# Kernel tuning notes

Hardware: AMD Instinct MI355X
Metric: run time of the kernel (lower is better)

Reference implementation:

```python
import jax, jax.numpy as jnp
import numpy as np

B, X_DIM, Y_DIM, HIDDEN = 512, 768, 128, 1024
H2 = HIDDEN // 2


def setup_inputs() -> dict:
    key = jax.random.key(0)
    ks = jax.random.split(key, 10)
    s_in = 1.0 / np.sqrt(X_DIM)
    s_h = 1.0 / np.sqrt(H2)
    return {
        "x_samples": jax.random.normal(ks[0], (B, X_DIM), jnp.float32),
        "y_samples": jax.random.normal(ks[1], (B, Y_DIM), jnp.float32),
        "w1_mu": jax.random.uniform(ks[2], (X_DIM, H2), jnp.float32, -s_in, s_in),
        "b1_mu": jax.random.uniform(ks[3], (H2,), jnp.float32, -s_in, s_in),
        "w2_mu": jax.random.uniform(ks[4], (H2, Y_DIM), jnp.float32, -s_h, s_h),
        "b2_mu": jax.random.uniform(ks[5], (Y_DIM,), jnp.float32, -s_h, s_h),
        "w1_lv": jax.random.uniform(ks[6], (X_DIM, H2), jnp.float32, -s_in, s_in),
        "b1_lv": jax.random.uniform(ks[7], (H2,), jnp.float32, -s_in, s_in),
        "w2_lv": jax.random.uniform(ks[8], (H2, Y_DIM), jnp.float32, -s_h, s_h),
        "b2_lv": jax.random.uniform(ks[9], (Y_DIM,), jnp.float32, -s_h, s_h),
    }


def reference(x_samples, y_samples, w1_mu, b1_mu, w2_mu, b2_mu,
              w1_lv, b1_lv, w2_lv, b2_lv):
    batch = y_samples.shape[0]
    # p_mu / p_logvar MLP heads
    mu = jax.nn.relu(x_samples @ w1_mu + b1_mu) @ w2_mu + b2_mu          # [B, Y]
    logvar = jnp.tanh(jax.nn.relu(x_samples @ w1_lv + b1_lv) @ w2_lv + b2_lv)  # [B, Y]

    inv_var = jnp.exp(-logvar)
    # positive: diagonal Gaussian log-prob of y_i under p(.|x_i), up to const
    positive = (-0.5 * (mu - y_samples) ** 2 * inv_var - 0.5 * logvar).sum(-1)  # [B]

    # pairwise log-probs: row i = params from x_i, col j = sample y_j
    mu_1 = mu[:, None, :]            # [B, 1, Y]
    lv_1 = logvar[:, None, :]        # [B, 1, Y]
    y_1 = y_samples[None, :, :]      # [1, B, Y]
    all_probs = (-0.5 * (y_1 - mu_1) ** 2 * jnp.exp(-lv_1) - 0.5 * lv_1).sum(-1)  # [B, B]

    # Faithful replication of the torch broadcasting: diag_mask is [B, B, 1],
    # so all_probs + diag_mask broadcasts to [B, B, B], then logsumexp over dim 0.
    diag_mask = (jnp.eye(batch, dtype=all_probs.dtype) * -20.0)[:, :, None]  # [B, B, 1]
    logits = all_probs + diag_mask                                           # [B, B, B]
    negative = jax.scipy.special.logsumexp(logits, axis=0) - jnp.log(batch - 1.0)  # [B, B]

    return (positive - negative).mean()
```

## Files before the change

### kernel.cpp

```cpp
#include <hip/hip_runtime.h>
#include <math.h>

#define BSZ   512
#define XD    768
#define YD    128
#define H2D   512

__global__ __launch_bounds__(256, 2) void layer1_kernel(
    const float* __restrict__ x,
    const float* __restrict__ w1_mu, const float* __restrict__ w1_lv,
    const float* __restrict__ y,
    float* __restrict__ p1,
    double* __restrict__ Sy, double* __restrict__ Sy2,
    double* __restrict__ accum, unsigned int* __restrict__ counter)
{
    __shared__ float As[16][68];
    __shared__ float Bs[16][68];
    const int t = threadIdx.x;

    if (blockIdx.z == 4) {
        const int id = blockIdx.x + 8 * blockIdx.y;
        if (id >= 16) return;
        const int dl = t & 7;
        const int g  = t >> 3;
        const int d  = id * 8 + dl;
        float s = 0.f, s2 = 0.f;
        for (int i = g * 16; i < g * 16 + 16; ++i) {
            const float v = y[i * YD + d];
            s += v; s2 += v * v;
        }
        float* shs  = &As[0][0];
        float* shs2 = &Bs[0][0];
        shs[t] = s; shs2[t] = s2;
        __syncthreads();
        if (t < 8) {
            double S = 0.0, S2 = 0.0;
            #pragma unroll
            for (int gg = 0; gg < 32; ++gg) {
                S += (double)shs[gg * 8 + t]; S2 += (double)shs2[gg * 8 + t];
            }
            Sy[id * 8 + t] = S; Sy2[id * 8 + t] = S2;
        } else if (id == 0 && t == 8)  { accum[0] = 0.0; }
        else if (id == 0 && t == 9)  { accum[1] = 0.0; }
        else if (id == 0 && t == 10) { *counter = 0u; }
        return;
    }

    const int bz     = blockIdx.z;
    const int branch = bz >> 1;
    const int ks     = bz & 1;
    const float* __restrict__ W = branch ? w1_lv : w1_mu;
    float* __restrict__ out = p1 + (size_t)bz * (BSZ * H2D);

    const int m0 = blockIdx.x * 64;
    const int n0 = blockIdx.y * 64;
    const int tx = t & 15;
    const int ty = t >> 4;

    const int am  = t >> 2;
    const int akq = (t & 3) << 2;
    const int bkk = t >> 4;
    const int bnq = (t & 15) << 2;

    const int kbase = ks * 384;
    float acc[4][4] = {};

    float4 a_pref = *(const float4*)&x[(m0 + am) * XD + kbase + akq];
    float4 b_pref = *(const float4*)&W[(kbase + bkk) * H2D + n0 + bnq];

    for (int kt = 0; kt < 384; kt += 16) {
        __syncthreads();
        As[akq + 0][am] = a_pref.x;
        As[akq + 1][am] = a_pref.y;
        As[akq + 2][am] = a_pref.z;
        As[akq + 3][am] = a_pref.w;
        *(float4*)&Bs[bkk][bnq] = b_pref;
        __syncthreads();
        if (kt + 16 < 384) {
            const int kn = kbase + kt + 16;
            a_pref = *(const float4*)&x[(m0 + am) * XD + kn + akq];
            b_pref = *(const float4*)&W[(kn + bkk) * H2D + n0 + bnq];
        }
        #pragma unroll
        for (int k = 0; k < 16; ++k) {
            const float4 av = *(const float4*)&As[k][ty * 4];
            const float4 bv = *(const float4*)&Bs[k][tx * 4];
            acc[0][0] += av.x*bv.x; acc[0][1] += av.x*bv.y; acc[0][2] += av.x*bv.z; acc[0][3] += av.x*bv.w;
            acc[1][0] += av.y*bv.x; acc[1][1] += av.y*bv.y; acc[1][2] += av.y*bv.z; acc[1][3] += av.y*bv.w;
            acc[2][0] += av.z*bv.x; acc[2][1] += av.z*bv.y; acc[2][2] += av.z*bv.z; acc[2][3] += av.z*bv.w;
            acc[3][0] += av.w*bv.x; acc[3][1] += av.w*bv.y; acc[3][2] += av.w*bv.z; acc[3][3] += av.w*bv.w;
        }
    }

    #pragma unroll
    for (int i = 0; i < 4; ++i) {
        const float4 o = make_float4(acc[i][0], acc[i][1], acc[i][2], acc[i][3]);
        *(float4*)&out[(m0 + ty * 4 + i) * H2D + n0 + tx * 4] = o;
    }
}

__global__ __launch_bounds__(256, 2) void layer2_kernel(
    const float* __restrict__ p1,
    const float* __restrict__ b1_mu, const float* __restrict__ b1_lv,
    const float* __restrict__ w2_mu, const float* __restrict__ w2_lv,
    float* __restrict__ p2)
{
    __shared__ float As[16][68];
    __shared__ float Bs[16][68];
    const int t = threadIdx.x;

    const int branch = blockIdx.z >> 3;
    const int ks     = blockIdx.z & 7;
    const float* __restrict__ pa = p1 + (size_t)(branch * 2 + 0) * (BSZ * H2D);
    const float* __restrict__ pb = p1 + (size_t)(branch * 2 + 1) * (BSZ * H2D);
    const float* __restrict__ b1 = branch ? b1_lv : b1_mu;
    const float* __restrict__ W  = branch ? w2_lv : w2_mu;
    float* __restrict__ out = p2 + (size_t)blockIdx.z * (BSZ * YD);

    const int m0 = blockIdx.x * 64;
    const int n0 = blockIdx.y * 64;
    const int tx = t & 15;
    const int ty = t >> 4;

    const int am  = t >> 2;
    const int akq = (t & 3) << 2;
    const int bkk = t >> 4;
    const int bnq = (t & 15) << 2;

    const int kbase = ks * 64;
    float acc[4][4] = {};

    float4 pa4 = *(const float4*)&pa[(m0 + am) * H2D + kbase + akq];
    float4 pb4 = *(const float4*)&pb[(m0 + am) * H2D + kbase + akq];
    float4 bb4 = *(const float4*)&b1[kbase + akq];
    float4 w4  = *(const float4*)&W[(kbase + bkk) * YD + n0 + bnq];

    for (int kt = 0; kt < 64; kt += 16) {
        __syncthreads();
        As[akq + 0][am] = fmaxf(pa4.x + pb4.x + bb4.x, 0.f);
        As[akq + 1][am] = fmaxf(pa4.y + pb4.y + bb4.y, 0.f);
        As[akq + 2][am] = fmaxf(pa4.z + pb4.z + bb4.z, 0.f);
        As[akq + 3][am] = fmaxf(pa4.w + pb4.w + bb4.w, 0.f);
        *(float4*)&Bs[bkk][bnq] = w4;
        __syncthreads();
        if (kt + 16 < 64) {
            const int kn = kbase + kt + 16;
            pa4 = *(const float4*)&pa[(m0 + am) * H2D + kn + akq];
            pb4 = *(const float4*)&pb[(m0 + am) * H2D + kn + akq];
            bb4 = *(const float4*)&b1[kn + akq];
            w4  = *(const float4*)&W[(kn + bkk) * YD + n0 + bnq];
        }
        #pragma unroll
        for (int k = 0; k < 16; ++k) {
            const float4 av = *(const float4*)&As[k][ty * 4];
            const float4 bv = *(const float4*)&Bs[k][tx * 4];
            acc[0][0] += av.x*bv.x; acc[0][1] += av.x*bv.y; acc[0][2] += av.x*bv.z; acc[0][3] += av.x*bv.w;
            acc[1][0] += av.y*bv.x; acc[1][1] += av.y*bv.y; acc[1][2] += av.y*bv.z; acc[1][3] += av.y*bv.w;
            acc[2][0] += av.z*bv.x; acc[2][1] += av.z*bv.y; acc[2][2] += av.z*bv.z; acc[2][3] += av.z*bv.w;
            acc[3][0] += av.w*bv.x; acc[3][1] += av.w*bv.y; acc[3][2] += av.w*bv.z; acc[3][3] += av.w*bv.w;
        }
    }

    #pragma unroll
    for (int i = 0; i < 4; ++i) {
        const float4 o = make_float4(acc[i][0], acc[i][1], acc[i][2], acc[i][3]);
        *(float4*)&out[(m0 + ty * 4 + i) * YD + n0 + tx * 4] = o;
    }
}

__global__ __launch_bounds__(256) void reduce_kernel(
    const float* __restrict__ p2, const float* __restrict__ y,
    const float* __restrict__ b2_mu, const float* __restrict__ b2_lv,
    const double* __restrict__ Sy, const double* __restrict__ Sy2,
    double* __restrict__ accum, unsigned int* __restrict__ counter,
    float* __restrict__ outp)
{
    const int NE = BSZ * YD;
    const int e  = blockIdx.x * 256 + threadIdx.x;
    const int d  = e & (YD - 1);

    float mu = b2_mu[d];
    float lp = b2_lv[d];
    #pragma unroll
    for (int s = 0; s < 8; ++s) {
        mu += p2[s * NE + e];
        lp += p2[(8 + s) * NE + e];
    }
    const float lv = tanhf(lp);
    const float iv = expf(-lv);
    const float dm = mu - y[e];

    double pos = -0.5 * (double)dm * (double)dm * (double)iv - 0.5 * (double)lv;
    double ap  = (double)iv * (-0.5 * Sy2[d] + (double)mu * Sy[d]
                               - 256.0 * (double)mu * (double)mu)
               - 256.0 * (double)lv;

    #pragma unroll
    for (int off = 32; off > 0; off >>= 1) {
        pos += __shfl_down(pos, off);
        ap  += __shfl_down(ap, off);
    }
    __shared__ double sp[4];
    __shared__ double sa[4];
    const int lane = threadIdx.x & 63;
    const int wv   = threadIdx.x >> 6;
    if (lane == 0) { sp[wv] = pos; sa[wv] = ap; }
    __syncthreads();
    if (threadIdx.x == 0) {
        atomicAdd(&accum[0], sp[0] + sp[1] + sp[2] + sp[3]);
        atomicAdd(&accum[1], sa[0] + sa[1] + sa[2] + sa[3]);
        __threadfence();
        const unsigned int old = atomicAdd(counter, 1u);
        if (old == 255u) {
            const double P = atomicAdd(&accum[0], 0.0);
            const double A = atomicAdd(&accum[1], 0.0);
            const double C = log1p(exp(-20.0) / 511.0);
            outp[0] = (float)(P / 512.0 - A / 262144.0 - C);
        }
    }
}

extern "C" void kernel_launch(void* const* d_in, const int* in_sizes, int n_in,
                              void* d_out, int out_size, void* d_ws, size_t ws_size,
                              hipStream_t stream) {
    const float* x     = (const float*)d_in[0];
    const float* y     = (const float*)d_in[1];
    const float* w1_mu = (const float*)d_in[2];
    const float* b1_mu = (const float*)d_in[3];
    const float* w2_mu = (const float*)d_in[4];
    const float* b2_mu = (const float*)d_in[5];
    const float* w1_lv = (const float*)d_in[6];
    const float* b1_lv = (const float*)d_in[7];
    const float* w2_lv = (const float*)d_in[8];
    const float* b2_lv = (const float*)d_in[9];

    char* ws = (char*)d_ws;
    float*  p1 = (float*)(ws);
    float*  p2 = (float*)(ws + (size_t)4 * BSZ * H2D * 4);
    double* Sy = (double*)(ws + (size_t)4 * BSZ * H2D * 4
                              + (size_t)16 * BSZ * YD * 4);
    double* Sy2 = Sy + YD;
    double* accum = Sy2 + YD;
    unsigned int* counter = (unsigned int*)(accum + 2);

    layer1_kernel<<<dim3(8, 8, 5), 256, 0, stream>>>(
        x, w1_mu, w1_lv, y, p1, Sy, Sy2, accum, counter);
    layer2_kernel<<<dim3(8, 2, 16), 256, 0, stream>>>(
        p1, b1_mu, b1_lv, w2_mu, w2_lv, p2);
    reduce_kernel<<<256, 256, 0, stream>>>(
        p2, y, b2_mu, b2_lv, Sy, Sy2, accum, counter, (float*)d_out);
}
```

Baseline: 110.5 us.

## Split layer-1 K dimension four ways and spread final atomics over slots

Layer 1 now splits the 768-long reduction into four 192-long partial products per branch instead of two, doubling the block count from 256 to 512 to fill more compute units. Layer 2 sums four partial planes instead of two when applying bias and ReLU, so it reads more intermediate data. The reduce kernel spreads its double-precision atomic adds across 16 slots to cut contention, and the last block sums the slots. The cost is a larger workspace and more global traffic for the intermediate buffers.

```diff
diff --git a/kernel.cpp b/kernel.cpp
--- a/kernel.cpp
+++ b/kernel.cpp
@@ -18,7 +18,7 @@
     __shared__ float Bs[16][68];
     const int t = threadIdx.x;
 
-    if (blockIdx.z == 4) {
+    if (blockIdx.z == 8) {
         const int id = blockIdx.x + 8 * blockIdx.y;
         if (id >= 16) return;
         const int dl = t & 7;
@@ -40,15 +40,14 @@
                 S += (double)shs[gg * 8 + t]; S2 += (double)shs2[gg * 8 + t];
             }
             Sy[id * 8 + t] = S; Sy2[id * 8 + t] = S2;
-        } else if (id == 0 && t == 8)  { accum[0] = 0.0; }
-        else if (id == 0 && t == 9)  { accum[1] = 0.0; }
-        else if (id == 0 && t == 10) { *counter = 0u; }
+        } else if (id == 0 && t >= 8 && t < 40) { accum[t - 8] = 0.0; }
+        else if (id == 0 && t == 40)            { *counter = 0u; }
         return;
     }
 
     const int bz     = blockIdx.z;
-    const int branch = bz >> 1;
-    const int ks     = bz & 1;
+    const int branch = bz >> 2;
+    const int ks     = bz & 3;
     const float* __restrict__ W = branch ? w1_lv : w1_mu;
     float* __restrict__ out = p1 + (size_t)bz * (BSZ * H2D);
 
@@ -62,13 +61,13 @@
     const int bkk = t >> 4;
     const int bnq = (t & 15) << 2;
 
-    const int kbase = ks * 384;
+    const int kbase = ks * 192;
     float acc[4][4] = {};
 
     float4 a_pref = *(const float4*)&x[(m0 + am) * XD + kbase + akq];
     float4 b_pref = *(const float4*)&W[(kbase + bkk) * H2D + n0 + bnq];
 
-    for (int kt = 0; kt < 384; kt += 16) {
+    for (int kt = 0; kt < 192; kt += 16) {
         __syncthreads();
         As[akq + 0][am] = a_pref.x;
         As[akq + 1][am] = a_pref.y;
@@ -76,7 +75,7 @@
         As[akq + 3][am] = a_pref.w;
         *(float4*)&Bs[bkk][bnq] = b_pref;
         __syncthreads();
-        if (kt + 16 < 384) {
+        if (kt + 16 < 192) {
             const int kn = kbase + kt + 16;
             a_pref = *(const float4*)&x[(m0 + am) * XD + kn + akq];
             b_pref = *(const float4*)&W[(kn + bkk) * H2D + n0 + bnq];
@@ -111,8 +110,10 @@
 
     const int branch = blockIdx.z >> 3;
     const int ks     = blockIdx.z & 7;
-    const float* __restrict__ pa = p1 + (size_t)(branch * 2 + 0) * (BSZ * H2D);
-    const float* __restrict__ pb = p1 + (size_t)(branch * 2 + 1) * (BSZ * H2D);
+    const float* __restrict__ pa = p1 + (size_t)(branch * 4 + 0) * (BSZ * H2D);
+    const float* __restrict__ pb = p1 + (size_t)(branch * 4 + 1) * (BSZ * H2D);
+    const float* __restrict__ pc = p1 + (size_t)(branch * 4 + 2) * (BSZ * H2D);
+    const float* __restrict__ pd = p1 + (size_t)(branch * 4 + 3) * (BSZ * H2D);
     const float* __restrict__ b1 = branch ? b1_lv : b1_mu;
     const float* __restrict__ W  = branch ? w2_lv : w2_mu;
     float* __restrict__ out = p2 + (size_t)blockIdx.z * (BSZ * YD);
@@ -132,21 +133,25 @@
 
     float4 pa4 = *(const float4*)&pa[(m0 + am) * H2D + kbase + akq];
     float4 pb4 = *(const float4*)&pb[(m0 + am) * H2D + kbase + akq];
+    float4 pc4 = *(const float4*)&pc[(m0 + am) * H2D + kbase + akq];
+    float4 pd4 = *(const float4*)&pd[(m0 + am) * H2D + kbase + akq];
     float4 bb4 = *(const float4*)&b1[kbase + akq];
     float4 w4  = *(const float4*)&W[(kbase + bkk) * YD + n0 + bnq];
 
     for (int kt = 0; kt < 64; kt += 16) {
         __syncthreads();
-        As[akq + 0][am] = fmaxf(pa4.x + pb4.x + bb4.x, 0.f);
-        As[akq + 1][am] = fmaxf(pa4.y + pb4.y + bb4.y, 0.f);
-        As[akq + 2][am] = fmaxf(pa4.z + pb4.z + bb4.z, 0.f);
-        As[akq + 3][am] = fmaxf(pa4.w + pb4.w + bb4.w, 0.f);
+        As[akq + 0][am] = fmaxf(pa4.x + pb4.x + pc4.x + pd4.x + bb4.x, 0.f);
+        As[akq + 1][am] = fmaxf(pa4.y + pb4.y + pc4.y + pd4.y + bb4.y, 0.f);
+        As[akq + 2][am] = fmaxf(pa4.z + pb4.z + pc4.z + pd4.z + bb4.z, 0.f);
+        As[akq + 3][am] = fmaxf(pa4.w + pb4.w + pc4.w + pd4.w + bb4.w, 0.f);
         *(float4*)&Bs[bkk][bnq] = w4;
         __syncthreads();
         if (kt + 16 < 64) {
             const int kn = kbase + kt + 16;
             pa4 = *(const float4*)&pa[(m0 + am) * H2D + kn + akq];
             pb4 = *(const float4*)&pb[(m0 + am) * H2D + kn + akq];
+            pc4 = *(const float4*)&pc[(m0 + am) * H2D + kn + akq];
+            pd4 = *(const float4*)&pd[(m0 + am) * H2D + kn + akq];
             bb4 = *(const float4*)&b1[kn + akq];
             w4  = *(const float4*)&W[(kn + bkk) * YD + n0 + bnq];
         }
@@ -202,18 +207,28 @@
     }
     __shared__ double sp[4];
     __shared__ double sa[4];
+    __shared__ double fin[32];
+    __shared__ int lastflag;
     const int lane = threadIdx.x & 63;
     const int wv   = threadIdx.x >> 6;
     if (lane == 0) { sp[wv] = pos; sa[wv] = ap; }
     __syncthreads();
     if (threadIdx.x == 0) {
-        atomicAdd(&accum[0], sp[0] + sp[1] + sp[2] + sp[3]);
-        atomicAdd(&accum[1], sa[0] + sa[1] + sa[2] + sa[3]);
+        const int slot = blockIdx.x & 15;
+        atomicAdd(&accum[slot],      sp[0] + sp[1] + sp[2] + sp[3]);
+        atomicAdd(&accum[16 + slot], sa[0] + sa[1] + sa[2] + sa[3]);
         __threadfence();
-        const unsigned int old = atomicAdd(counter, 1u);
-        if (old == 255u) {
-            const double P = atomicAdd(&accum[0], 0.0);
-            const double A = atomicAdd(&accum[1], 0.0);
+        lastflag = (atomicAdd(counter, 1u) == 255u) ? 1 : 0;
+    }
+    __syncthreads();
+    if (lastflag) {
+        if (threadIdx.x < 32)
+            fin[threadIdx.x] = atomicAdd(&accum[threadIdx.x], 0.0);
+        __syncthreads();
+        if (threadIdx.x == 0) {
+            double P = 0.0, A = 0.0;
+            #pragma unroll
+            for (int s = 0; s < 16; ++s) { P += fin[s]; A += fin[16 + s]; }
             const double C = log1p(exp(-20.0) / 511.0);
             outp[0] = (float)(P / 512.0 - A / 262144.0 - C);
         }
@@ -236,14 +251,14 @@
 
     char* ws = (char*)d_ws;
     float*  p1 = (float*)(ws);
-    float*  p2 = (float*)(ws + (size_t)4 * BSZ * H2D * 4);
-    double* Sy = (double*)(ws + (size_t)4 * BSZ * H2D * 4
+    float*  p2 = (float*)(ws + (size_t)8 * BSZ * H2D * 4);
+    double* Sy = (double*)(ws + (size_t)8 * BSZ * H2D * 4
                               + (size_t)16 * BSZ * YD * 4);
     double* Sy2 = Sy + YD;
     double* accum = Sy2 + YD;
-    unsigned int* counter = (unsigned int*)(accum + 2);
-
-    layer1_kernel<<<dim3(8, 8, 5), 256, 0, stream>>>(
+    unsigned int* counter = (unsigned int*)(accum + 32);
+
+    layer1_kernel<<<dim3(8, 8, 9), 256, 0, stream>>>(
         x, w1_mu, w1_lv, y, p1, Sy, Sy2, accum, counter);
     layer2_kernel<<<dim3(8, 2, 16), 256, 0, stream>>>(
         p1, b1_mu, b1_lv, w2_mu, w2_lv, p2);
```

New measurement: 104.7 us. 1.05x faster.
